# Optimization experiments

Measured on AMD Instinct MI355X. Metric: run time of the kernel, lower is better.

Reference implementation:

```python
import jax, jax.numpy as jnp
import numpy as np

DIM = 512
HEADS = 16
WH, WW = 8, 8
N = WH * WW
B_ = 1024
NW = 64
CPB_HID = 512


def setup_inputs() -> dict:
    key = jax.random.key(0)
    ks = jax.random.split(key, 10)
    x = jax.random.normal(ks[0], (B_, N, DIM), dtype=jnp.float32)
    # 0 / -100 shifted-window style additive mask (finite stand-in for -inf)
    mask = jnp.where(jax.random.uniform(ks[1], (NW, N, N)) < 0.1, -100.0, 0.0).astype(jnp.float32)
    qkv_w = jax.random.normal(ks[2], (DIM, 3 * DIM), dtype=jnp.float32) * 0.02
    q_bias = jnp.zeros((DIM,), jnp.float32)
    v_bias = jnp.zeros((DIM,), jnp.float32)
    logit_scale = jnp.log(10.0 * jnp.ones((1, HEADS, 1, 1), jnp.float32))
    cpb_w1 = jax.random.normal(ks[3], (2, CPB_HID), dtype=jnp.float32) * 0.02
    cpb_b1 = jnp.zeros((CPB_HID,), jnp.float32)
    cpb_w2 = jax.random.normal(ks[4], (CPB_HID, HEADS), dtype=jnp.float32) * 0.02
    proj_w = jax.random.normal(ks[5], (DIM, DIM), dtype=jnp.float32) * 0.02
    proj_b = jnp.zeros((DIM,), jnp.float32)
    return dict(x=x, mask=mask, qkv_w=qkv_w, q_bias=q_bias, v_bias=v_bias,
                logit_scale=logit_scale, cpb_w1=cpb_w1, cpb_b1=cpb_b1,
                cpb_w2=cpb_w2, proj_w=proj_w, proj_b=proj_b)


def _coords_table():
    # continuous relative coords table, normalized/log-scaled as in Swin-V2
    rel_h = jnp.arange(-(WH - 1), WH, dtype=jnp.float32)
    rel_w = jnp.arange(-(WW - 1), WW, dtype=jnp.float32)
    t = jnp.stack(jnp.meshgrid(rel_h, rel_w), axis=-1)  # (2Ww-1, 2Wh-1, 2)
    t = t / jnp.array([WH - 1, WW - 1], dtype=jnp.float32)
    t = t * 8.0
    t = jnp.sign(t) * jnp.log2(jnp.abs(t) + 1.0) / jnp.log2(jnp.float32(8.0))
    return t.reshape(-1, 2)  # ((2Wh-1)*(2Ww-1), 2)


def _rel_pos_index():
    ch = jnp.arange(WH)
    cw = jnp.arange(WW)
    coords = jnp.stack(jnp.meshgrid(ch, cw))          # (2, Ww, Wh), xy indexing
    cf = coords.reshape(2, -1)                        # (2, N)
    rel = cf[:, :, None] - cf[:, None, :]             # (2, N, N)
    ry = (rel[0] + WH - 1) * (2 * WW - 1)
    rx = rel[1] + WW - 1
    return (ry + rx).reshape(-1)                      # (N*N,) int


def reference(x, mask, qkv_w, q_bias, v_bias, logit_scale, cpb_w1, cpb_b1, cpb_w2, proj_w, proj_b):
    Bw, n, C = x.shape
    hd = C // HEADS
    # qkv with bias = [q_bias, 0, v_bias]
    qkv_bias = jnp.concatenate([q_bias, jnp.zeros_like(v_bias), v_bias])
    qkv = x @ qkv_w + qkv_bias                        # (B_, N, 3C)
    qkv = qkv.reshape(Bw, n, 3, HEADS, hd).transpose(2, 0, 3, 1, 4)
    q, k, v = qkv[0], qkv[1], qkv[2]                  # (B_, H, N, hd)
    # cosine attention
    qn = q / jnp.linalg.norm(q, axis=-1, keepdims=True)
    kn = k / jnp.linalg.norm(k, axis=-1, keepdims=True)
    attn = jnp.einsum('bhnd,bhmd->bhnm', qn, kn)
    scale = jnp.exp(jnp.minimum(logit_scale, jnp.log(jnp.float32(100.0))))
    attn = attn * scale
    # continuous position bias: MLP(table) then gather by relative index
    table = _coords_table()
    bias_table = jax.nn.relu(table @ cpb_w1 + cpb_b1) @ cpb_w2   # (T, H)
    rpb = bias_table[_rel_pos_index()].reshape(n, n, HEADS).transpose(2, 0, 1)
    rpb = 16.0 * jax.nn.sigmoid(rpb)
    attn = attn + rpb[None]                           # (B_, H, N, N)
    # shifted-window mask
    nW = mask.shape[0]
    attn = attn.reshape(Bw // nW, nW, HEADS, n, n) + mask[None, :, None]
    attn = attn.reshape(Bw, HEADS, n, n)
    attn = jax.nn.softmax(attn, axis=-1)
    out = jnp.einsum('bhnm,bhmd->bhnd', attn, v)
    out = out.transpose(0, 2, 1, 3).reshape(Bw, n, C)
    return out @ proj_w + proj_b
```

## Files before the change

kernel.cpp:

```cpp
#include <hip/hip_runtime.h>
#include <cstdint>

typedef unsigned short u16;
typedef float    f32x4  __attribute__((ext_vector_type(4)));
typedef __bf16   bf16x8 __attribute__((ext_vector_type(8)));
typedef unsigned int u32x4 __attribute__((ext_vector_type(4)));

#define DIMC   512
#define HEADS  16
#define NTOK   64
#define BWIN   1024
#define HD     32
#define QKV_ONE (1024u*16u*64u*32u)

__device__ __forceinline__ u16 f2bf(float x) {
  unsigned u = __float_as_uint(x);
  u += 0x7FFFu + ((u >> 16) & 1u);
  return (u16)(u >> 16);
}
__device__ __forceinline__ float bf2f(u16 h) {
  return __uint_as_float(((unsigned)h) << 16);
}
__device__ __forceinline__ void gld16(const u16* g, u16* l) {
  __builtin_amdgcn_global_load_lds((const __attribute__((address_space(1))) void*)g,
                                   (__attribute__((address_space(3))) void*)l, 16, 0, 0);
}

__global__ void cpb_kernel(const float* __restrict__ w1, const float* __restrict__ b1,
                           const float* __restrict__ w2, float* __restrict__ table) {
  int t  = blockIdx.x;
  int ti = t / 15, tj = t % 15;
  float v0 = (float)(tj - 7) * (8.0f / 7.0f);
  float v1 = (float)(ti - 7) * (8.0f / 7.0f);
  float c0 = copysignf(log2f(fabsf(v0) + 1.0f) / 3.0f, v0);
  float c1 = copysignf(log2f(fabsf(v1) + 1.0f) / 3.0f, v1);
  float acc[HEADS];
#pragma unroll
  for (int h = 0; h < HEADS; ++h) acc[h] = 0.f;
  for (int k = threadIdx.x; k < 512; k += 64) {
    float hid = fmaxf(c0 * w1[k] + c1 * w1[512 + k] + b1[k], 0.0f);
#pragma unroll
    for (int h = 0; h < HEADS; ++h) acc[h] += hid * w2[k * HEADS + h];
  }
#pragma unroll
  for (int off = 32; off >= 1; off >>= 1) {
#pragma unroll
    for (int h = 0; h < HEADS; ++h) acc[h] += __shfl_xor(acc[h], off, 64);
  }
  if (threadIdx.x == 0) {
#pragma unroll
    for (int h = 0; h < HEADS; ++h) table[t * HEADS + h] = acc[h];
  }
}

__global__ void cbias_kernel(const float* __restrict__ table, const float* __restrict__ mask,
                             float* __restrict__ cbias) {
  int wh = blockIdx.x; int w = wh >> 4, h = wh & 15;
  const float* mrow = mask + (size_t)w * 4096;
  float* crow = cbias + (size_t)wh * 4096;
  for (int e = threadIdx.x; e < 4096; e += blockDim.x) {
    int i = e >> 6, j = e & 63;
    int dh = (i & 7) - (j & 7);
    int dw = (i >> 3) - (j >> 3);
    int idx = (dh + 7) * 15 + (dw + 7);
    float r = table[idx * HEADS + h];
    float rpb = 16.0f / (1.0f + __expf(-r));
    crow[e] = rpb + mrow[e];
  }
}

__global__ void cast_x_kernel(const float* __restrict__ src, u16* __restrict__ dst, int n8) {
  int i = blockIdx.x * blockDim.x + threadIdx.x;
  if (i >= n8) return;
  const f32x4* s4 = (const f32x4*)src;
  f32x4 a = s4[(size_t)2 * i], b = s4[(size_t)2 * i + 1];
  u16 o[8];
#pragma unroll
  for (int j = 0; j < 4; ++j) { o[j] = f2bf(a[j]); o[4 + j] = f2bf(b[j]); }
  *(u32x4*)(dst + (size_t)i * 8) = *(const u32x4*)o;
}

__global__ void tcast_kernel(const float* __restrict__ w, u16* __restrict__ wt, int K, int N) {
  int i = blockIdx.x * blockDim.x + threadIdx.x;
  if (i >= K * N) return;
  int n = i / K, k = i % K;
  wt[i] = f2bf(w[(size_t)k * N + n]);
}

#define STAGE(slot) do {                                           \
    u16* _sb = lds + (slot) * 16384;                               \
    gld16(ga, _sb + aW);                                           \
    gld16(ga + (size_t)16 * K, _sb + aW + 16 * 32);                \
    gld16(gb, _sb + 8192 + aW);                                    \
    gld16(gb + (size_t)16 * K, _sb + 8192 + aW + 16 * 32);         \
    ga += 32; gb += 32; } while (0)

#define COMPUTE(slot) do {                                         \
    const u16* _cb = lds + (slot) * 16384;                         \
    bf16x8 afr[8], bfr[4];                                         \
    _Pragma("unroll")                                              \
    for (int mt = 0; mt < 8; ++mt) afr[mt] = *(const bf16x8*)(_cb + aoff[mt]); \
    _Pragma("unroll")                                              \
    for (int nt = 0; nt < 4; ++nt) bfr[nt] = *(const bf16x8*)(_cb + boff[nt]); \
    __builtin_amdgcn_s_setprio(1);                                 \
    _Pragma("unroll")                                              \
    for (int mt = 0; mt < 8; ++mt)                                 \
      _Pragma("unroll")                                            \
      for (int nt = 0; nt < 4; ++nt)                               \
        acc[mt][nt] = __builtin_amdgcn_mfma_f32_16x16x32_bf16(afr[mt], bfr[nt], acc[mt][nt], 0, 0, 0); \
    __builtin_amdgcn_s_setprio(0); } while (0)

#define WAITB(n) do {                                              \
    asm volatile("s_waitcnt vmcnt(" #n ")" ::: "memory");          \
    __builtin_amdgcn_s_barrier();                                  \
    asm volatile("" ::: "memory"); } while (0)

template <int EPI>
__global__ __launch_bounds__(512, 2) void gemm8_kernel(
    const u16* __restrict__ A, const u16* __restrict__ Bt,
    const float* __restrict__ bias0, const float* __restrict__ bias1,
    void* __restrict__ outp, int M, int N, int K) {
  extern __shared__ u16 lds[];
  const int nb = N >> 8;
  const int cpx = gridDim.x >> 3;
  const int bid = blockIdx.x;
  const int wg = (bid & 7) * cpx + (bid >> 3);
  const int m0 = (wg / nb) << 8;
  const int n0 = (wg % nb) << 8;
  const int tid = threadIdx.x, lane = tid & 63, wid = tid >> 6;
  const int wm = wid >> 2, wn = wid & 3;
  const int quad = lane >> 4, li = lane & 15;

  const int srow = lane >> 2;
  const int scol = ((lane & 3) ^ (srow & 3)) << 3;
  const u16* ga = A  + (size_t)(m0 + wid * 32 + srow) * K + scol;
  const u16* gb = Bt + (size_t)(n0 + wid * 32 + srow) * K + scol;
  const int aW = wid * 32 * 32;

  int aoff[8], boff[4];
#pragma unroll
  for (int mt = 0; mt < 8; ++mt)
    aoff[mt] = (wm * 128 + mt * 16 + li) * 32 + ((quad ^ (li & 3)) << 3);
#pragma unroll
  for (int nt = 0; nt < 4; ++nt)
    boff[nt] = 8192 + (wn * 64 + nt * 16 + li) * 32 + ((quad ^ (li & 3)) << 3);

  const f32x4 z = {0.f, 0.f, 0.f, 0.f};
  f32x4 acc[8][4];
#pragma unroll
  for (int i = 0; i < 8; ++i)
#pragma unroll
    for (int j = 0; j < 4; ++j) acc[i][j] = z;

  STAGE(0); STAGE(1); STAGE(2);
  WAITB(8);

  const int KT = K >> 5;
  for (int t = 0; t < KT - 3; ++t) {
    STAGE((t + 3) & 3);
    COMPUTE(t & 3);
    WAITB(8);
  }
  COMPUTE((KT - 3) & 3);
  WAITB(4);
  COMPUTE((KT - 2) & 3);
  WAITB(0);
  COMPUTE((KT - 1) & 3);

  if (EPI == 0) {
    u16* qkvp = (u16*)outp;
#pragma unroll
    for (int nt = 0; nt < 4; ++nt) {
      int n = n0 + wn * 64 + nt * 16 + li;
      float bv = (n < 512) ? bias0[n] : ((n < 1024) ? 0.f : bias1[n - 1024]);
      int three = n >> 9, h = (n >> 5) & 15, d = n & 31;
#pragma unroll
      for (int mt = 0; mt < 8; ++mt) {
#pragma unroll
        for (int r = 0; r < 4; ++r) {
          int m = m0 + wm * 128 + mt * 16 + quad * 4 + r;
          int b = m >> 6, tk = m & 63;
          size_t dst = (size_t)three * QKV_ONE + (((size_t)(b * 16 + h) * 64 + tk) * 32) + d;
          qkvp[dst] = f2bf(acc[mt][nt][r] + bv);
        }
      }
    }
  } else {
    float* op = (float*)outp;
#pragma unroll
    for (int nt = 0; nt < 4; ++nt) {
      int n = n0 + wn * 64 + nt * 16 + li;
      float bv = bias0[n];
#pragma unroll
      for (int mt = 0; mt < 8; ++mt) {
#pragma unroll
        for (int r = 0; r < 4; ++r) {
          int m = m0 + wm * 128 + mt * 16 + quad * 4 + r;
          op[(size_t)m * N + n] = acc[mt][nt][r] + bv;
        }
      }
    }
  }
}

__global__ __launch_bounds__(256, 2) void attn_kernel(
    const u16* __restrict__ qkv, const float* __restrict__ cbias,
    const float* __restrict__ lsc, u16* __restrict__ attn_out) {
  __shared__ u16 qs[64 * 40], ks[64 * 40];
  __shared__ u16 vt[32 * 72];
  __shared__ u16 ps[64 * 72];
  __shared__ float invq[64], invk[64];
  const int bid = blockIdx.x;
  const int b = bid >> 4, h = bid & 15;
  const int tid = threadIdx.x, lane = tid & 63, wid = tid >> 6;
  const int quad = lane >> 4, li = lane & 15;
  const size_t base = (size_t)(b * HEADS + h) * (64 * 32);
  const u16* qp = qkv + base;
  const u16* kp = qp + (size_t)QKV_ONE;
  const u16* vp = qp + (size_t)2 * QKV_ONE;
  {
    int r = tid >> 2, c = (tid & 3) * 8;
    u32x4 q4 = *(const u32x4*)(qp + r * 32 + c);
    u32x4 k4 = *(const u32x4*)(kp + r * 32 + c);
    u32x4 v4 = *(const u32x4*)(vp + r * 32 + c);
    *(u32x4*)(qs + r * 40 + c) = q4;
    *(u32x4*)(ks + r * 40 + c) = k4;
    u16 tmp[8];
    *(u32x4*)tmp = v4;
#pragma unroll
    for (int j = 0; j < 8; ++j) vt[(c + j) * 72 + r] = tmp[j];
  }
  __syncthreads();
  if (tid < 128) {
    int r = tid & 63;
    const u16* src = (tid < 64) ? qs : ks;
    float s = 0.f;
#pragma unroll
    for (int d = 0; d < 32; ++d) { float x = bf2f(src[r * 40 + d]); s += x * x; }
    float inv = rsqrtf(s);
    if (tid < 64) invq[r] = inv; else invk[r] = inv;
  }
  __syncthreads();

  const float scale = __expf(fminf(lsc[h], 4.6051701859880914f));

  const f32x4 z = {0.f, 0.f, 0.f, 0.f};
  f32x4 sacc[4] = {z, z, z, z};
  bf16x8 qa = *(const bf16x8*)(qs + (wid * 16 + li) * 40 + quad * 8);
#pragma unroll
  for (int nt = 0; nt < 4; ++nt) {
    bf16x8 kb = *(const bf16x8*)(ks + (nt * 16 + li) * 40 + quad * 8);
    sacc[nt] = __builtin_amdgcn_mfma_f32_16x16x32_bf16(qa, kb, sacc[nt], 0, 0, 0);
  }
  const float* cb = cbias + ((size_t)(b & 63) * HEADS + h) * 4096;
  float lg[4][4];
#pragma unroll
  for (int nt = 0; nt < 4; ++nt) {
#pragma unroll
    for (int r = 0; r < 4; ++r) {
      int row = wid * 16 + quad * 4 + r;
      int col = nt * 16 + li;
      lg[nt][r] = sacc[nt][r] * invq[row] * invk[col] * scale + cb[row * 64 + col];
    }
  }
#pragma unroll
  for (int r = 0; r < 4; ++r) {
    float mx = fmaxf(fmaxf(lg[0][r], lg[1][r]), fmaxf(lg[2][r], lg[3][r]));
#pragma unroll
    for (int off = 1; off < 16; off <<= 1) mx = fmaxf(mx, __shfl_xor(mx, off, 64));
    float e[4], s = 0.f;
#pragma unroll
    for (int nt = 0; nt < 4; ++nt) { e[nt] = __expf(lg[nt][r] - mx); s += e[nt]; }
#pragma unroll
    for (int off = 1; off < 16; off <<= 1) s += __shfl_xor(s, off, 64);
    float rs = 1.0f / s;
    int row = wid * 16 + quad * 4 + r;
#pragma unroll
    for (int nt = 0; nt < 4; ++nt) ps[row * 72 + nt * 16 + li] = f2bf(e[nt] * rs);
  }
  f32x4 oacc[2] = {z, z};
#pragma unroll
  for (int kc = 0; kc < 2; ++kc) {
    bf16x8 pa = *(const bf16x8*)(ps + (wid * 16 + li) * 72 + kc * 32 + quad * 8);
#pragma unroll
    for (int nt = 0; nt < 2; ++nt) {
      bf16x8 vb = *(const bf16x8*)(vt + (nt * 16 + li) * 72 + kc * 32 + quad * 8);
      oacc[nt] = __builtin_amdgcn_mfma_f32_16x16x32_bf16(pa, vb, oacc[nt], 0, 0, 0);
    }
  }
  u16* op = attn_out + ((size_t)b * 64) * DIMC + h * HD;
#pragma unroll
  for (int nt = 0; nt < 2; ++nt) {
#pragma unroll
    for (int r = 0; r < 4; ++r) {
      int row = wid * 16 + quad * 4 + r;
      op[(size_t)row * DIMC + nt * 16 + li] = f2bf(oacc[nt][r]);
    }
  }
}

extern "C" void kernel_launch(void* const* d_in, const int* in_sizes, int n_in,
                              void* d_out, int out_size, void* d_ws, size_t ws_size,
                              hipStream_t stream) {
  const float* x    = (const float*)d_in[0];
  const float* mask = (const float*)d_in[1];
  const float* qkvw = (const float*)d_in[2];
  const float* qb   = (const float*)d_in[3];
  const float* vb   = (const float*)d_in[4];
  const float* lsc  = (const float*)d_in[5];
  const float* w1   = (const float*)d_in[6];
  const float* b1   = (const float*)d_in[7];
  const float* w2   = (const float*)d_in[8];
  const float* pw   = (const float*)d_in[9];
  const float* pb   = (const float*)d_in[10];
  float* out = (float*)d_out;

  char* ws = (char*)d_ws;
  u16*   x_bf    = (u16*)(ws);
  u16*   qkv_bf  = (u16*)(ws + 67108864);
  u16*   attn_o  = x_bf;
  u16*   wqkv_t  = (u16*)(ws + 268435456);
  u16*   wproj_t = (u16*)(ws + 270008320);
  float* table   = (float*)(ws + 270532608);
  float* cbias   = (float*)(ws + 270548992);

  static int inited = 0;
  if (!inited) {
    hipFuncSetAttribute(reinterpret_cast<const void*>(&gemm8_kernel<0>),
                        hipFuncAttributeMaxDynamicSharedMemorySize, 131072);
    hipFuncSetAttribute(reinterpret_cast<const void*>(&gemm8_kernel<1>),
                        hipFuncAttributeMaxDynamicSharedMemorySize, 131072);
    inited = 1;
  }

  cpb_kernel<<<225, 64, 0, stream>>>(w1, b1, w2, table);
  cbias_kernel<<<1024, 256, 0, stream>>>(table, mask, cbias);
  cast_x_kernel<<<16384, 256, 0, stream>>>(x, x_bf, 65536 * 512 / 8);
  tcast_kernel<<<3072, 256, 0, stream>>>(qkvw, wqkv_t, 512, 1536);
  tcast_kernel<<<1024, 256, 0, stream>>>(pw, wproj_t, 512, 512);
  gemm8_kernel<0><<<1536, 512, 131072, stream>>>(x_bf, wqkv_t, qb, vb, qkv_bf, 65536, 1536, 512);
  attn_kernel<<<16384, 256, 0, stream>>>(qkv_bf, cbias, lsc, attn_o);
  gemm8_kernel<1><<<512, 512, 131072, stream>>>(attn_o, wproj_t, pb, nullptr, out, 65536, 512, 512);
}
```

Before: 549.7 us.

## Split GEMM k-step into two MFMA halves interleaved with staged loads and barriers

The GEMM main loop now splits each k-tile into two halves of four M-subtiles. The A and B global-to-LDS loads are issued between them, with extra barriers and explicit lgkmcnt waits, in a ping-pong style. This should overlap memory issue with MFMA work and lower register pressure by holding only four A fragments at a time. The LDS swizzle also changes from (li&3) to ((li>>1)&3) to reduce bank conflicts on fragment reads. The cost is more barriers per k-tile, which could serialize the waves.

```diff
diff --git a/kernel.cpp b/kernel.cpp
--- a/kernel.cpp
+++ b/kernel.cpp
@@ -87,33 +87,48 @@
   wt[i] = f2bf(w[(size_t)k * N + n]);
 }
 
-#define STAGE(slot) do {                                           \
-    u16* _sb = lds + (slot) * 16384;                               \
-    gld16(ga, _sb + aW);                                           \
-    gld16(ga + (size_t)16 * K, _sb + aW + 16 * 32);                \
-    gld16(gb, _sb + 8192 + aW);                                    \
-    gld16(gb + (size_t)16 * K, _sb + 8192 + aW + 16 * 32);         \
-    ga += 32; gb += 32; } while (0)
-
-#define COMPUTE(slot) do {                                         \
-    const u16* _cb = lds + (slot) * 16384;                         \
-    bf16x8 afr[8], bfr[4];                                         \
-    _Pragma("unroll")                                              \
-    for (int mt = 0; mt < 8; ++mt) afr[mt] = *(const bf16x8*)(_cb + aoff[mt]); \
-    _Pragma("unroll")                                              \
+#define STAGE_A(slot) do { u16* _sa = lds + (slot) * 16384;            \
+    gld16(ga, _sa + aW); gld16(ga + (size_t)16 * K, _sa + aW + 512);   \
+    ga += 32; } while (0)
+#define STAGE_B(slot) do { u16* _sbb = lds + (slot) * 16384 + 8192;    \
+    gld16(gb, _sbb + aW); gld16(gb + (size_t)16 * K, _sbb + aW + 512); \
+    gb += 32; } while (0)
+#define VM(n) asm volatile("s_waitcnt vmcnt(" #n ")" ::: "memory")
+#define NOPX ((void)0)
+
+#define TILE(slot, SA, SB, WN) do {                                    \
+    const u16* _cb = lds + (slot) * 16384;                             \
+    bf16x8 afr[4], bfr[4];                                             \
+    _Pragma("unroll")                                                  \
+    for (int mt = 0; mt < 4; ++mt) afr[mt] = *(const bf16x8*)(_cb + aoff[mt]); \
+    _Pragma("unroll")                                                  \
     for (int nt = 0; nt < 4; ++nt) bfr[nt] = *(const bf16x8*)(_cb + boff[nt]); \
-    __builtin_amdgcn_s_setprio(1);                                 \
-    _Pragma("unroll")                                              \
-    for (int mt = 0; mt < 8; ++mt)                                 \
-      _Pragma("unroll")                                            \
-      for (int nt = 0; nt < 4; ++nt)                               \
+    SA;                                                                \
+    __builtin_amdgcn_s_barrier();                                      \
+    asm volatile("s_waitcnt lgkmcnt(0)" ::: "memory");                 \
+    __builtin_amdgcn_s_setprio(1);                                     \
+    _Pragma("unroll")                                                  \
+    for (int mt = 0; mt < 4; ++mt)                                     \
+      _Pragma("unroll")                                                \
+      for (int nt = 0; nt < 4; ++nt)                                   \
         acc[mt][nt] = __builtin_amdgcn_mfma_f32_16x16x32_bf16(afr[mt], bfr[nt], acc[mt][nt], 0, 0, 0); \
-    __builtin_amdgcn_s_setprio(0); } while (0)
-
-#define WAITB(n) do {                                              \
-    asm volatile("s_waitcnt vmcnt(" #n ")" ::: "memory");          \
-    __builtin_amdgcn_s_barrier();                                  \
-    asm volatile("" ::: "memory"); } while (0)
+    __builtin_amdgcn_s_setprio(0);                                     \
+    __builtin_amdgcn_s_barrier();                                      \
+    _Pragma("unroll")                                                  \
+    for (int mt = 0; mt < 4; ++mt) afr[mt] = *(const bf16x8*)(_cb + aoff[4 + mt]); \
+    SB;                                                                \
+    __builtin_amdgcn_s_barrier();                                      \
+    asm volatile("s_waitcnt lgkmcnt(0)" ::: "memory");                 \
+    __builtin_amdgcn_s_setprio(1);                                     \
+    _Pragma("unroll")                                                  \
+    for (int mt = 0; mt < 4; ++mt)                                     \
+      _Pragma("unroll")                                                \
+      for (int nt = 0; nt < 4; ++nt)                                   \
+        acc[4 + mt][nt] = __builtin_amdgcn_mfma_f32_16x16x32_bf16(afr[mt], bfr[nt], acc[4 + mt][nt], 0, 0, 0); \
+    __builtin_amdgcn_s_setprio(0);                                     \
+    WN;                                                                \
+    __builtin_amdgcn_s_barrier();                                      \
+  } while (0)
 
 template <int EPI>
 __global__ __launch_bounds__(512, 2) void gemm8_kernel(
@@ -132,7 +147,7 @@
   const int quad = lane >> 4, li = lane & 15;
 
   const int srow = lane >> 2;
-  const int scol = ((lane & 3) ^ (srow & 3)) << 3;
+  const int scol = ((lane & 3) ^ ((lane >> 3) & 3)) << 3;
   const u16* ga = A  + (size_t)(m0 + wid * 32 + srow) * K + scol;
   const u16* gb = Bt + (size_t)(n0 + wid * 32 + srow) * K + scol;
   const int aW = wid * 32 * 32;
@@ -140,10 +155,10 @@
   int aoff[8], boff[4];
 #pragma unroll
   for (int mt = 0; mt < 8; ++mt)
-    aoff[mt] = (wm * 128 + mt * 16 + li) * 32 + ((quad ^ (li & 3)) << 3);
+    aoff[mt] = (wm * 128 + mt * 16 + li) * 32 + ((quad ^ ((li >> 1) & 3)) << 3);
 #pragma unroll
   for (int nt = 0; nt < 4; ++nt)
-    boff[nt] = 8192 + (wn * 64 + nt * 16 + li) * 32 + ((quad ^ (li & 3)) << 3);
+    boff[nt] = 8192 + (wn * 64 + nt * 16 + li) * 32 + ((quad ^ ((li >> 1) & 3)) << 3);
 
   const f32x4 z = {0.f, 0.f, 0.f, 0.f};
   f32x4 acc[8][4];
@@ -152,20 +167,17 @@
 #pragma unroll
     for (int j = 0; j < 4; ++j) acc[i][j] = z;
 
-  STAGE(0); STAGE(1); STAGE(2);
-  WAITB(8);
+  STAGE_A(0); STAGE_B(0); STAGE_A(1); STAGE_B(1); STAGE_A(2); STAGE_B(2);
+  VM(8);
+  __builtin_amdgcn_s_barrier();
 
   const int KT = K >> 5;
   for (int t = 0; t < KT - 3; ++t) {
-    STAGE((t + 3) & 3);
-    COMPUTE(t & 3);
-    WAITB(8);
-  }
-  COMPUTE((KT - 3) & 3);
-  WAITB(4);
-  COMPUTE((KT - 2) & 3);
-  WAITB(0);
-  COMPUTE((KT - 1) & 3);
+    TILE(t & 3, STAGE_A((t + 3) & 3), STAGE_B((t + 3) & 3), VM(8));
+  }
+  TILE((KT - 3) & 3, NOPX, NOPX, VM(4));
+  TILE((KT - 2) & 3, NOPX, NOPX, VM(0));
+  TILE((KT - 1) & 3, NOPX, NOPX, NOPX);
 
   if (EPI == 0) {
     u16* qkvp = (u16*)outp;
```

Measured after the change: 541.8 us. About the same (-1.4%).
